# Kernel tuning notes

Hardware: AMD Instinct MI355X
Metric: run time of the kernel (lower is better)

The kernel has to match this reference:

```python
import jax, jax.numpy as jnp
import numpy as np

DINO_SHIFT = 0.7
COEF = 1.0
EPS = 1e-12


def setup_inputs() -> dict:
    key = jax.random.key(0)
    k1, k2 = jax.random.split(key)
    N, H, W, C, K = 2, 48, 48, 384, 16
    dino_feature_map = jax.random.normal(k1, (N, H, W, C), dtype=jnp.float32)
    # relevance map in log space (log-probabilities over classes)
    log_p_class = jax.nn.log_softmax(jax.random.normal(k2, (N, H, W, K), dtype=jnp.float32), axis=-1)
    dino_pos_weight = jnp.ones((1,), dtype=jnp.float32)
    dino_neg_weight = jnp.ones((1,), dtype=jnp.float32)
    return {
        "dino_feature_map": dino_feature_map,
        "log_p_class": log_p_class,
        "dino_pos_weight": dino_pos_weight,
        "dino_neg_weight": dino_neg_weight,
    }


def _normalize(x):
    # F.normalize(x, dim=-1): x / max(||x||, eps)
    n = jnp.sqrt(jnp.sum(x * x, axis=-1, keepdims=True))
    return x / jnp.maximum(n, EPS)


def _js_correlation(a, b):
    # a, b: [N, L, C] log-probs. Pairwise JS divergence matrix [N, L, L].
    # Same math as the torch broadcast version, but the sum over C is
    # factored into einsums so the [N,L,L,C] tensor is never materialized:
    #   kl_am[s,l] = sum_c e^{a[s,c]} a[s,c] - sum_c e^{a[s,c]} m[l,c]
    m = jnp.logaddexp(a, b) - jnp.log(2.0)           # [N, L, C]
    ea = jnp.exp(a)
    kl_am = jnp.sum(ea * a, axis=-1)[:, :, None] - jnp.einsum('nsc,nlc->nsl', ea, m)
    eb = jnp.exp(b)
    kl_bm = jnp.sum(eb * b, axis=-1)[:, :, None] - jnp.einsum('nsc,nlc->nsl', eb, m)
    return (kl_am + kl_bm) / 2.0


def _fda_loss(feats, log_p, pw, nw):
    N = feats.shape[0]
    f = feats.reshape(N, -1, feats.shape[-1])          # [N, HW, C]
    p = log_p.reshape(N, -1, log_p.shape[-1])          # [N, HW, K]
    fn = _normalize(f)
    f_corr = jnp.einsum('nsc,nlc->nsl', fn, fn) - DINO_SHIFT
    f_corr = jax.lax.stop_gradient(f_corr)             # torch.no_grad block
    f_pos = jnp.maximum(f_corr, 0.0)
    f_neg = jnp.minimum(f_corr, 0.0)
    p_corr = _js_correlation(p, p)                     # [N, HW, HW]
    n_pos = jnp.count_nonzero(f_pos).astype(f_pos.dtype)
    n_neg = jnp.count_nonzero(f_neg).astype(f_neg.dtype)
    pos_loss = jnp.sum(f_pos * p_corr) / n_pos
    neg_loss = jnp.sum(f_neg * p_corr) / n_neg
    loss = pos_loss * pw[0] + neg_loss * nw[0]
    return loss * COEF                                 # reduction='none' on a scalar


def reference(dino_feature_map, log_p_class, dino_pos_weight, dino_neg_weight):
    return _fda_loss(dino_feature_map, log_p_class, dino_pos_weight, dino_neg_weight)
```

## Files before the change

### kernel.cpp

```cpp
#include <hip/hip_runtime.h>
#include <math.h>
#include <stdint.h>

#define NN 2
#define LL 2304
#define CC 384
#define KK 16
#define DINO_SHIFT 0.7f

#define NT 24
#define TB 96
#define TT ((NT * (NT + 1)) / 2)
#define NBLK2 (NN * TT)

typedef __attribute__((ext_vector_type(8))) short short8;
typedef __attribute__((ext_vector_type(4))) float f32x4;
typedef __attribute__((ext_vector_type(2))) float f32x2;

#define AS_G __attribute__((address_space(1)))
#define AS_L __attribute__((address_space(3)))

__device__ __forceinline__ unsigned short f2bf(float x) {
    union { float f; uint32_t u; } v; v.f = x;
    uint32_t r = v.u + 0x7fffu + ((v.u >> 16) & 1u);
    return (unsigned short)(r >> 16);
}

__device__ __forceinline__ unsigned int f2e4m3(float x) {
    unsigned int u = __float_as_uint(x);
    unsigned int s = (u >> 24) & 0x80u;
    unsigned int au = u & 0x7fffffffu;
    unsigned int code;
    if (au < 0x3C800000u) {
        code = (unsigned int)__builtin_rintf(__uint_as_float(au) * 512.0f);
    } else {
        unsigned int lsb = (au >> 20) & 1u;
        au += 0x7FFFFu + lsb;
        code = (au >> 20) - (120u << 3);
    }
    return s | code;
}
__device__ __forceinline__ unsigned short fp8pair(float a, float b) {
#if __has_builtin(__builtin_amdgcn_cvt_pk_fp8_f32)
    return (unsigned short)(__builtin_amdgcn_cvt_pk_fp8_f32(a, b, 0, false) & 0xffff);
#else
    return (unsigned short)(f2e4m3(a) | (f2e4m3(b) << 8));
#endif
}

__device__ __forceinline__ void gll16(const void* g, void* l) {
    __builtin_amdgcn_global_load_lds((const AS_G unsigned int*)g,
                                     (AS_L unsigned int*)l, 16, 0, 0);
}

__global__ void prep_kernel(const float* __restrict__ f, const float* __restrict__ p,
                            unsigned char* __restrict__ fnorm8,
                            unsigned short* __restrict__ Ppad,
                            unsigned short* __restrict__ ppad,
                            float* __restrict__ selfdot) {
    const int r = blockIdx.x * 4 + (threadIdx.x >> 6);
    const int lane = threadIdx.x & 63;
    const f32x2* frow2 = (const f32x2*)(f + (size_t)r * CC);
    f32x2 v[3];
    float ss = 0.f;
#pragma unroll
    for (int k = 0; k < 3; ++k) {
        v[k] = frow2[lane + 64 * k];
        ss = fmaf(v[k][0], v[k][0], fmaf(v[k][1], v[k][1], ss));
    }
#pragma unroll
    for (int off = 32; off; off >>= 1) ss += __shfl_xor(ss, off);
    const float rn = 1.0f / fmaxf(sqrtf(ss), 1e-12f);
    unsigned short* fr = (unsigned short*)(fnorm8 + (size_t)r * CC);
#pragma unroll
    for (int k = 0; k < 3; ++k)
        fr[lane + 64 * k] = fp8pair(v[k][0] * rn, v[k][1] * rn);

    if (lane < 32) {
        float pv = 0.f, e = 0.f;
        if (lane < KK) { pv = p[(size_t)r * KK + lane]; e = expf(pv); }
        Ppad[(size_t)r * 32 + lane] = (lane < KK) ? f2bf(e)  : (unsigned short)0;
        ppad[(size_t)r * 32 + lane] = (lane < KK) ? f2bf(pv) : (unsigned short)0;
        float sd = e * pv;
#pragma unroll
        for (int off = 8; off; off >>= 1) sd += __shfl_xor(sd, off, 16);
        if (lane == 0) selfdot[r] = sd;
    }
}

__global__ __launch_bounds__(256, 2) void pair_kernel(
    const unsigned char* __restrict__ fnorm8,
    const unsigned short* __restrict__ Ppad, const unsigned short* __restrict__ ppad,
    const float* __restrict__ selfdot, float* __restrict__ partials)
{
    __shared__ char lds[49152] __attribute__((aligned(16)));
    __shared__ float red[4][4];

    const int b = blockIdx.x;
    const int n = b / TT;
    int t = b % TT;
    int i = 0;
    while (t >= NT - i) { t -= NT - i; ++i; }
    const int j = i + t;
    const int s0 = i * TB, l0 = j * TB;
    const float wgt = (i == j) ? 1.f : 2.f;

    const int tid = threadIdx.x, lane = tid & 63, w = tid >> 6;
    const int wrow = w >> 1, wcol = w & 1;

    const unsigned char* fn = fnorm8 + (size_t)n * LL * CC;
    const int srow8 = lane >> 3, sch = lane & 7;

    f32x4 acc[3][3] = {};

    auto stageF = [&](int buf, int kt) {
        char* base = lds + buf * 24576;
#pragma unroll
        for (int q = 0; q < 3; ++q) {
            const int r0 = w * 24 + q * 8;
            const int row = r0 + srow8;
            const int swz = (sch ^ (row & 7)) << 4;
            gll16(fn + (size_t)(s0 + row) * CC + kt * 128 + swz, base + r0 * 128);
            gll16(fn + (size_t)(l0 + row) * CC + kt * 128 + swz,
                  base + 12288 + r0 * 128);
        }
    };
    auto stagePP = [&]() {
        const char* Pb = (const char*)Ppad + (size_t)(n * LL + s0) * 64;
        const char* pb = (const char*)ppad + (size_t)(n * LL + l0) * 64;
        const int erow = lane >> 2, ech = lane & 3;
#pragma unroll
        for (int q3 = 0; q3 < 3; ++q3) {
            const int q = w * 3 + q3;
            const int qq = (q < 6) ? q : q - 6;
            const int row = qq * 16 + erow;
            const char* sb = (q < 6) ? Pb : pb;
            gll16(sb + row * 64 + ((ech ^ (row & 3)) << 4),
                  lds + ((q < 6) ? 24576 : 30720) + qq * 1024);
        }
    };
    auto compute = [&](int buf) {
        const char* abase = lds + buf * 24576;
        const char* bbase = abase + 12288;
#pragma unroll
        for (int ks = 0; ks < 4; ++ks) {
            long a[3], bb[3];
            const int unit = ks * 2 + ((lane >> 5) & 1);
            const int w8 = ((lane >> 4) & 1) * 8;
#pragma unroll
            for (int im = 0; im < 3; ++im) {
                const int row = wrow * 48 + im * 16 + (lane & 15);
                a[im] = *(const long*)(abase + row * 128
                         + ((unit ^ (row & 7)) << 4) + w8);
            }
#pragma unroll
            for (int jn = 0; jn < 3; ++jn) {
                const int row = wcol * 48 + jn * 16 + (lane & 15);
                bb[jn] = *(const long*)(bbase + row * 128
                         + ((unit ^ (row & 7)) << 4) + w8);
            }
#pragma unroll
            for (int im = 0; im < 3; ++im)
#pragma unroll
                for (int jn = 0; jn < 3; ++jn)
                    acc[im][jn] = __builtin_amdgcn_mfma_f32_16x16x32_fp8_fp8(
                        a[im], bb[jn], acc[im][jn], 0, 0, 0);
        }
    };

    stageF(0, 0);
    stageF(1, 1);
    asm volatile("s_waitcnt vmcnt(6)" ::: "memory");
    asm volatile("s_barrier" ::: "memory");
    compute(0);
    asm volatile("s_barrier" ::: "memory");
    stageF(0, 2);
    asm volatile("s_waitcnt vmcnt(6)" ::: "memory");
    asm volatile("s_barrier" ::: "memory");
    compute(1);
    asm volatile("s_barrier" ::: "memory");
    stagePP();
    asm volatile("s_waitcnt vmcnt(3)" ::: "memory");
    asm volatile("s_barrier" ::: "memory");
    compute(0);
    asm volatile("s_barrier" ::: "memory");
    asm volatile("s_waitcnt vmcnt(0)" ::: "memory");
    asm volatile("s_barrier" ::: "memory");

    short8 a2[3], b2[3];
#pragma unroll
    for (int im = 0; im < 3; ++im) {
        const int row = wrow * 48 + im * 16 + (lane & 15);
        a2[im] = *(const short8*)(lds + 24576 + row * 64
                  + (((lane >> 4) ^ (row & 3)) << 4));
    }
#pragma unroll
    for (int jn = 0; jn < 3; ++jn) {
        const int row = wcol * 48 + jn * 16 + (lane & 15);
        b2[jn] = *(const short8*)(lds + 30720 + row * 64
                  + (((lane >> 4) ^ (row & 3)) << 4));
    }

    float pos = 0.f, neg = 0.f, npc = 0.f, nnc = 0.f;
#pragma unroll
    for (int im = 0; im < 3; ++im) {
        const f32x4 sd4 = *(const f32x4*)(selfdot + (size_t)n * LL + s0
                            + wrow * 48 + im * 16 + ((lane >> 4) << 2));
#pragma unroll
        for (int jn = 0; jn < 3; ++jn) {
            f32x4 z = {0.f, 0.f, 0.f, 0.f};
            f32x4 pdv = __builtin_amdgcn_mfma_f32_16x16x32_bf16(a2[im], b2[jn], z, 0, 0, 0);
#pragma unroll
            for (int r = 0; r < 4; ++r) {
                const float fc = acc[im][jn][r] - DINO_SHIFT;
                const float pc = sd4[r] - pdv[r];
                const float v = fc * pc;
                if (fc > 0.f)      { pos += v; npc += 1.f; }
                else if (fc < 0.f) { neg += v; nnc += 1.f; }
            }
        }
    }
    pos *= wgt; neg *= wgt; npc *= wgt; nnc *= wgt;

#pragma unroll
    for (int off = 32; off; off >>= 1) {
        pos += __shfl_xor(pos, off); neg += __shfl_xor(neg, off);
        npc += __shfl_xor(npc, off); nnc += __shfl_xor(nnc, off);
    }
    if (lane == 0) { red[w][0] = pos; red[w][1] = neg; red[w][2] = npc; red[w][3] = nnc; }
    __syncthreads();
    if (tid == 0) {
        partials[b * 4 + 0] = red[0][0] + red[1][0] + red[2][0] + red[3][0];
        partials[b * 4 + 1] = red[0][1] + red[1][1] + red[2][1] + red[3][1];
        partials[b * 4 + 2] = red[0][2] + red[1][2] + red[2][2] + red[3][2];
        partials[b * 4 + 3] = red[0][3] + red[1][3] + red[2][3] + red[3][3];
    }
}

__global__ void final_kernel(const float* __restrict__ partials,
                             const float* __restrict__ pw,
                             const float* __restrict__ nw,
                             float* __restrict__ out) {
    __shared__ float red[4][4];
    const int tid = threadIdx.x;
    float pos = 0.f, neg = 0.f, np = 0.f, nn = 0.f;
    for (int i = tid; i < NBLK2; i += 256) {
        const f32x4 v = *(const f32x4*)(partials + i * 4);
        pos += v[0]; neg += v[1]; np += v[2]; nn += v[3];
    }
#pragma unroll
    for (int off = 32; off; off >>= 1) {
        pos += __shfl_xor(pos, off); neg += __shfl_xor(neg, off);
        np  += __shfl_xor(np, off);  nn  += __shfl_xor(nn, off);
    }
    const int w = tid >> 6, lane = tid & 63;
    if (lane == 0) { red[w][0] = pos; red[w][1] = neg; red[w][2] = np; red[w][3] = nn; }
    __syncthreads();
    if (tid == 0) {
        pos = red[0][0] + red[1][0] + red[2][0] + red[3][0];
        neg = red[0][1] + red[1][1] + red[2][1] + red[3][1];
        np  = red[0][2] + red[1][2] + red[2][2] + red[3][2];
        nn  = red[0][3] + red[1][3] + red[2][3] + red[3][3];
        out[0] = (pos / np) * pw[0] + (neg / nn) * nw[0];
    }
}

extern "C" void kernel_launch(void* const* d_in, const int* in_sizes, int n_in,
                              void* d_out, int out_size, void* d_ws, size_t ws_size,
                              hipStream_t stream) {
    const float* f  = (const float*)d_in[0];
    const float* p  = (const float*)d_in[1];
    const float* pw = (const float*)d_in[2];
    const float* nw = (const float*)d_in[3];
    float* out = (float*)d_out;

    unsigned char* fnorm8 = (unsigned char*)d_ws;
    unsigned short* Ppad  = (unsigned short*)(fnorm8 + (size_t)NN * LL * CC);
    unsigned short* ppad  = Ppad + (size_t)NN * LL * 32;
    float* selfdot  = (float*)(ppad + (size_t)NN * LL * 32);
    float* partials = selfdot + (size_t)NN * LL;

    prep_kernel<<<(NN * LL) / 4, 256, 0, stream>>>(f, p, fnorm8, Ppad, ppad, selfdot);
    pair_kernel<<<NBLK2, 256, 0, stream>>>(fnorm8, Ppad, ppad, selfdot, partials);
    final_kernel<<<1, 256, 0, stream>>>(partials, pw, nw, out);
}
```

Baseline: 21.49 us.

## Load full feature tiles in one shot, dedupe diagonal B tile, read P directly

Replaces the three-stage double-buffered K pipeline with a single bulk load of the full 384-wide fp8 feature rows for both tiles into a larger LDS buffer (72 KB), followed by one barrier and an unpipelined compute loop. On diagonal tiles the B tile is skipped and A is reused. The bf16 probability fragments and selfdot are now loaded straight from global into registers instead of staged through LDS. This cuts barriers and waitcnt stalls and drops redundant loads on diagonal blocks, but the larger LDS footprint likely lowers occupancy (the 2 blocks per CU target may not fit) and removes overlap between loading and MFMA work.

Measured after the change: 25.33 us. 17.9% more time.

```diff
diff --git a/kernel.cpp b/kernel.cpp
--- a/kernel.cpp
+++ b/kernel.cpp
@@ -93,7 +93,7 @@
     const unsigned short* __restrict__ Ppad, const unsigned short* __restrict__ ppad,
     const float* __restrict__ selfdot, float* __restrict__ partials)
 {
-    __shared__ char lds[49152] __attribute__((aligned(16)));
+    __shared__ char lds[73728] __attribute__((aligned(16)));
     __shared__ float red[4][4];
 
     const int b = blockIdx.x;
@@ -103,60 +103,74 @@
     while (t >= NT - i) { t -= NT - i; ++i; }
     const int j = i + t;
     const int s0 = i * TB, l0 = j * TB;
-    const float wgt = (i == j) ? 1.f : 2.f;
+    const bool diag = (i == j);
+    const float wgt = diag ? 1.f : 2.f;
 
     const int tid = threadIdx.x, lane = tid & 63, w = tid >> 6;
     const int wrow = w >> 1, wcol = w & 1;
 
     const unsigned char* fn = fnorm8 + (size_t)n * LL * CC;
-    const int srow8 = lane >> 3, sch = lane & 7;
-
+
+#pragma unroll
+    for (int q = 0; q < 9; ++q) {
+        const int slot = tid + 256 * q;
+        const int row = slot / 24;
+        const int jj = slot % 24;
+        const int g = jj >> 3, c = jj & 7;
+        gll16(fn + (size_t)(s0 + row) * CC + g * 128 + ((c ^ (row & 7)) << 4),
+              lds + slot * 16);
+    }
+    if (!diag) {
+#pragma unroll
+        for (int q = 0; q < 9; ++q) {
+            const int slot = tid + 256 * q;
+            const int row = slot / 24;
+            const int jj = slot % 24;
+            const int g = jj >> 3, c = jj & 7;
+            gll16(fn + (size_t)(l0 + row) * CC + g * 128 + ((c ^ (row & 7)) << 4),
+                  lds + 36864 + slot * 16);
+        }
+    }
+
+    short8 a2[3], b2[3];
+    f32x4 sd4[3];
+#pragma unroll
+    for (int im = 0; im < 3; ++im) {
+        const int row = wrow * 48 + im * 16 + (lane & 15);
+        a2[im] = *(const short8*)((const char*)Ppad
+                  + (size_t)(n * LL + s0 + row) * 64 + ((lane >> 4) << 4));
+        sd4[im] = *(const f32x4*)(selfdot + (size_t)n * LL + s0
+                  + wrow * 48 + im * 16 + ((lane >> 4) << 2));
+    }
+#pragma unroll
+    for (int jn = 0; jn < 3; ++jn) {
+        const int row = wcol * 48 + jn * 16 + (lane & 15);
+        b2[jn] = *(const short8*)((const char*)ppad
+                  + (size_t)(n * LL + l0 + row) * 64 + ((lane >> 4) << 4));
+    }
+
+    __syncthreads();
+
+    const char* abase = lds;
+    const char* bbase = diag ? lds : lds + 36864;
     f32x4 acc[3][3] = {};
-
-    auto stageF = [&](int buf, int kt) {
-        char* base = lds + buf * 24576;
-#pragma unroll
-        for (int q = 0; q < 3; ++q) {
-            const int r0 = w * 24 + q * 8;
-            const int row = r0 + srow8;
-            const int swz = (sch ^ (row & 7)) << 4;
-            gll16(fn + (size_t)(s0 + row) * CC + kt * 128 + swz, base + r0 * 128);
-            gll16(fn + (size_t)(l0 + row) * CC + kt * 128 + swz,
-                  base + 12288 + r0 * 128);
-        }
-    };
-    auto stagePP = [&]() {
-        const char* Pb = (const char*)Ppad + (size_t)(n * LL + s0) * 64;
-        const char* pb = (const char*)ppad + (size_t)(n * LL + l0) * 64;
-        const int erow = lane >> 2, ech = lane & 3;
-#pragma unroll
-        for (int q3 = 0; q3 < 3; ++q3) {
-            const int q = w * 3 + q3;
-            const int qq = (q < 6) ? q : q - 6;
-            const int row = qq * 16 + erow;
-            const char* sb = (q < 6) ? Pb : pb;
-            gll16(sb + row * 64 + ((ech ^ (row & 3)) << 4),
-                  lds + ((q < 6) ? 24576 : 30720) + qq * 1024);
-        }
-    };
-    auto compute = [&](int buf) {
-        const char* abase = lds + buf * 24576;
-        const char* bbase = abase + 12288;
+#pragma unroll
+    for (int kt = 0; kt < 3; ++kt) {
 #pragma unroll
         for (int ks = 0; ks < 4; ++ks) {
-            long a[3], bb[3];
             const int unit = ks * 2 + ((lane >> 5) & 1);
             const int w8 = ((lane >> 4) & 1) * 8;
+            long a[3], bb[3];
 #pragma unroll
             for (int im = 0; im < 3; ++im) {
                 const int row = wrow * 48 + im * 16 + (lane & 15);
-                a[im] = *(const long*)(abase + row * 128
+                a[im] = *(const long*)(abase + row * 384 + kt * 128
                          + ((unit ^ (row & 7)) << 4) + w8);
             }
 #pragma unroll
             for (int jn = 0; jn < 3; ++jn) {
                 const int row = wcol * 48 + jn * 16 + (lane & 15);
-                bb[jn] = *(const long*)(bbase + row * 128
+                bb[jn] = *(const long*)(bbase + row * 384 + kt * 128
                          + ((unit ^ (row & 7)) << 4) + w8);
             }
 #pragma unroll
@@ -166,46 +180,11 @@
                     acc[im][jn] = __builtin_amdgcn_mfma_f32_16x16x32_fp8_fp8(
                         a[im], bb[jn], acc[im][jn], 0, 0, 0);
         }
-    };
-
-    stageF(0, 0);
-    stageF(1, 1);
-    asm volatile("s_waitcnt vmcnt(6)" ::: "memory");
-    asm volatile("s_barrier" ::: "memory");
-    compute(0);
-    asm volatile("s_barrier" ::: "memory");
-    stageF(0, 2);
-    asm volatile("s_waitcnt vmcnt(6)" ::: "memory");
-    asm volatile("s_barrier" ::: "memory");
-    compute(1);
-    asm volatile("s_barrier" ::: "memory");
-    stagePP();
-    asm volatile("s_waitcnt vmcnt(3)" ::: "memory");
-    asm volatile("s_barrier" ::: "memory");
-    compute(0);
-    asm volatile("s_barrier" ::: "memory");
-    asm volatile("s_waitcnt vmcnt(0)" ::: "memory");
-    asm volatile("s_barrier" ::: "memory");
-
-    short8 a2[3], b2[3];
+    }
+
+    float pos = 0.f, neg = 0.f, npc = 0.f, nnc = 0.f;
 #pragma unroll
     for (int im = 0; im < 3; ++im) {
-        const int row = wrow * 48 + im * 16 + (lane & 15);
-        a2[im] = *(const short8*)(lds + 24576 + row * 64
-                  + (((lane >> 4) ^ (row & 3)) << 4));
-    }
-#pragma unroll
-    for (int jn = 0; jn < 3; ++jn) {
-        const int row = wcol * 48 + jn * 16 + (lane & 15);
-        b2[jn] = *(const short8*)(lds + 30720 + row * 64
-                  + (((lane >> 4) ^ (row & 3)) << 4));
-    }
-
-    float pos = 0.f, neg = 0.f, npc = 0.f, nnc = 0.f;
-#pragma unroll
-    for (int im = 0; im < 3; ++im) {
-        const f32x4 sd4 = *(const f32x4*)(selfdot + (size_t)n * LL + s0
-                            + wrow * 48 + im * 16 + ((lane >> 4) << 2));
 #pragma unroll
         for (int jn = 0; jn < 3; ++jn) {
             f32x4 z = {0.f, 0.f, 0.f, 0.f};
@@ -213,7 +192,7 @@
 #pragma unroll
             for (int r = 0; r < 4; ++r) {
                 const float fc = acc[im][jn][r] - DINO_SHIFT;
-                const float pc = sd4[r] - pdv[r];
+                const float pc = sd4[im][r] - pdv[r];
                 const float v = fc * pc;
                 if (fc > 0.f)      { pos += v; npc += 1.f; }
                 else if (fc < 0.f) { neg += v; nnc += 1.f; }
```
